# Optimization experiments

Hardware: AMD Instinct MI355X
Metric: run time of the kernel (lower is better)

The kernel has to match this reference:

```python
import jax, jax.numpy as jnp
import numpy as np

N_HEAD = 16
D_MODEL = 1024
D_K = 64
D_V = 64
LN_EPS = 1e-5


def setup_inputs() -> dict:
    key = jax.random.key(0)
    ks = jax.random.split(key, 12)
    B, S = 8, 1024
    q = jax.random.normal(ks[0], (B, S, D_MODEL), jnp.float32)
    k = jax.random.normal(ks[1], (B, S, D_MODEL), jnp.float32)
    v = jax.random.normal(ks[2], (B, S, D_MODEL), jnp.float32)
    mask = jnp.zeros((B, S, S), jnp.bool_)
    std_qk = np.sqrt(2.0 / (D_MODEL + D_K)).astype(np.float32)
    std_v = np.sqrt(2.0 / (D_MODEL + D_V)).astype(np.float32)
    Wq = jax.random.normal(ks[3], (D_MODEL, N_HEAD * D_K), jnp.float32) * std_qk
    Wk = jax.random.normal(ks[4], (D_MODEL, N_HEAD * D_K), jnp.float32) * std_qk
    Wv = jax.random.normal(ks[5], (D_MODEL, N_HEAD * D_V), jnp.float32) * std_v
    bq = jnp.zeros((N_HEAD * D_K,), jnp.float32)
    bk = jnp.zeros((N_HEAD * D_K,), jnp.float32)
    bv = jnp.zeros((N_HEAD * D_V,), jnp.float32)
    Wo = jax.random.normal(ks[6], (N_HEAD * D_V, D_MODEL), jnp.float32) * np.sqrt(2.0 / (N_HEAD * D_V + D_MODEL)).astype(np.float32)
    bo = jnp.zeros((D_MODEL,), jnp.float32)
    gamma = jnp.ones((D_MODEL,), jnp.float32)
    beta = jnp.zeros((D_MODEL,), jnp.float32)
    return {"q": q, "k": k, "v": v, "mask": mask, "Wq": Wq, "bq": bq,
            "Wk": Wk, "bk": bk, "Wv": Wv, "bv": bv, "Wo": Wo, "bo": bo,
            "gamma": gamma, "beta": beta}


def reference(q, k, v, mask, Wq, bq, Wk, bk, Wv, bv, Wo, bo, gamma, beta):
    B, Lq, _ = q.shape
    Lk = k.shape[1]
    residual = q
    # QKV projections -> (B, L, H, dh)
    qh = (q @ Wq + bq).reshape(B, Lq, N_HEAD, D_K)
    kh = (k @ Wk + bk).reshape(B, Lk, N_HEAD, D_K)
    vh = (v @ Wv + bv).reshape(B, Lk, N_HEAD, D_V)
    temperature = jnp.sqrt(jnp.asarray(D_K, qh.dtype))
    # scores: (H, B, Lq, Lk) to match torch head-major (n_head*bsz) layout
    scores = jnp.einsum('bqhd,bkhd->hbqk', qh, kh) / temperature
    scores = jnp.where(mask[None, :, :, :], -jnp.inf, scores)
    attn = jax.nn.softmax(scores, axis=-1)  # dropout is identity in eval
    out = jnp.einsum('hbqk,bkhd->bqhd', attn, vh).reshape(B, Lq, N_HEAD * D_V)
    out = out @ Wo + bo  # output dropout identity in eval
    # layer norm over last dim with residual
    x = out + residual
    mu = jnp.mean(x, axis=-1, keepdims=True)
    var = jnp.var(x, axis=-1, keepdims=True)
    y = (x - mu) * jax.lax.rsqrt(var + LN_EPS) * gamma + beta
    return y, attn.reshape(N_HEAD * B, Lq, Lk)
```

## Files before the change

kernel.cpp:

```cpp
#include <hip/hip_runtime.h>
#include <cstdint>

using f4  = __attribute__((ext_vector_type(4))) float;
using s8v = __attribute__((ext_vector_type(8))) short;
using u4v = __attribute__((ext_vector_type(4))) unsigned short;
using u8v = __attribute__((ext_vector_type(8))) unsigned short;

typedef unsigned short ushort_t;
typedef unsigned int   uint_t;

__device__ __forceinline__ ushort_t f2bf(float f) {
  union { float f; uint_t u; } x; x.f = f;
  uint_t r = x.u + 0x7fffu + ((x.u >> 16) & 1u);
  return (ushort_t)(r >> 16);
}
__device__ __forceinline__ float bf2f(ushort_t h) {
  union { uint_t u; float f; } x; x.u = ((uint_t)h) << 16;
  return x.f;
}

__device__ __forceinline__ void gload16(const void* gptr, void* ldsptr) {
  __builtin_amdgcn_global_load_lds(
      (const __attribute__((address_space(1))) void*)gptr,
      (__attribute__((address_space(3))) void*)ldsptr, 16, 0, 0);
}

__device__ __forceinline__ s8v ldfrag(const ushort_t* lds, int row, int kh, int g) {
  int cb = ((kh * 64 + g * 16) ^ ((row & 7) << 4));
  return *(const s8v*)((const char*)lds + row * 128 + cb);
}
__device__ __forceinline__ void st_p(ushort_t* lds, int row, int colbyte, ushort_t v) {
  *(ushort_t*)((char*)lds + row * 128 + (colbyte ^ ((row & 7) << 4))) = v;
}

__global__ __launch_bounds__(256) void wtrans_k(
    const float* __restrict__ Wq, const float* __restrict__ Wk,
    const float* __restrict__ Wv, const float* __restrict__ Wo,
    ushort_t* __restrict__ WT)
{
  int z = blockIdx.z;
  const float* W = (z == 0) ? Wq : (z == 1) ? Wk : (z == 2) ? Wv : Wo;
  ushort_t* D = WT + (size_t)z * 1048576;
  int k0 = blockIdx.x * 64, n0 = blockIdx.y * 64;
  __shared__ float t[64][65];
  int tid = threadIdx.x;
  int r16 = tid >> 4, c4 = (tid & 15) * 4;
#pragma unroll
  for (int p = 0; p < 4; ++p) {
    int kk = p * 16 + r16;
    f4 vv = *(const f4*)(W + (size_t)(k0 + kk) * 1024 + n0 + c4);
#pragma unroll
    for (int j = 0; j < 4; ++j) t[kk][c4 + j] = vv[j];
  }
  __syncthreads();
#pragma unroll
  for (int p = 0; p < 4; ++p) {
    int nn = p * 16 + r16;
    u4v o;
#pragma unroll
    for (int j = 0; j < 4; ++j) o[j] = f2bf(t[c4 + j][nn]);
    *(u4v*)(D + (size_t)(n0 + nn) * 1024 + k0 + c4) = o;
  }
}

__global__ __launch_bounds__(256) void gemm3_k(
    const float* __restrict__ Aq, const float* __restrict__ Ak,
    const float* __restrict__ Av, const ushort_t* __restrict__ WTall,
    const float* __restrict__ bq, const float* __restrict__ bk,
    const float* __restrict__ bv,
    ushort_t* __restrict__ Qh, ushort_t* __restrict__ Kh, ushort_t* __restrict__ Vh)
{
  __shared__ ushort_t As[128 * 64];
  __shared__ ushort_t Bs[128 * 64];
  int z = blockIdx.z;
  const float* A     = (z == 0) ? Aq : (z == 1) ? Ak : Av;
  const ushort_t* BT = WTall + (size_t)z * 1048576;
  const float* bias  = (z == 0) ? bq : (z == 1) ? bk : bv;
  ushort_t* out      = (z == 0) ? Qh : (z == 1) ? Kh : Vh;

  int tid = threadIdx.x;
  int l = tid & 63, w = tid >> 6;
  int lr = l & 15, g = l >> 4;
  int wr = w >> 1, wc = w & 1;
  const int m0 = blockIdx.x * 128;
  const int n0 = blockIdx.y * 128;

  f4 acc[4][4];
#pragma unroll
  for (int i = 0; i < 4; ++i)
#pragma unroll
    for (int j = 0; j < 4; ++j) acc[i][j] = (f4){0.f, 0.f, 0.f, 0.f};

  const ushort_t* Bp = BT + (size_t)n0 * 1024;
  const int swz = ((l & 7) ^ (l >> 3)) * 8;
  const int rb = l >> 3;

  for (int k0 = 0; k0 < 1024; k0 += 64) {
    __syncthreads();
#pragma unroll
    for (int c = 0; c < 4; ++c) {
      int seg = c * 4 + w;
      gload16(Bp + (size_t)(seg * 8 + rb) * 1024 + k0 + swz, (void*)(Bs + seg * 512));
    }
#pragma unroll
    for (int c = 0; c < 4; ++c) {
      int seg = c * 4 + w;
      int row = seg * 8 + rb;
      const float* ap = A + (size_t)(m0 + row) * 1024 + k0 + swz;
      f4 a0 = *(const f4*)ap;
      f4 a1 = *(const f4*)(ap + 4);
      u8v o;
      o[0] = f2bf(a0[0]); o[1] = f2bf(a0[1]); o[2] = f2bf(a0[2]); o[3] = f2bf(a0[3]);
      o[4] = f2bf(a1[0]); o[5] = f2bf(a1[1]); o[6] = f2bf(a1[2]); o[7] = f2bf(a1[3]);
      *(u8v*)((char*)As + row * 128 + (l & 7) * 16) = o;
    }
    __syncthreads();
#pragma unroll
    for (int kh = 0; kh < 2; ++kh) {
      s8v af[4], bfr[4];
#pragma unroll
      for (int mt = 0; mt < 4; ++mt) af[mt] = ldfrag(As, wr * 64 + mt * 16 + lr, kh, g);
#pragma unroll
      for (int nt = 0; nt < 4; ++nt) bfr[nt] = ldfrag(Bs, wc * 64 + nt * 16 + lr, kh, g);
#pragma unroll
      for (int mt = 0; mt < 4; ++mt)
#pragma unroll
        for (int nt = 0; nt < 4; ++nt)
          acc[mt][nt] = __builtin_amdgcn_mfma_f32_16x16x32_bf16(af[mt], bfr[nt], acc[mt][nt], 0, 0, 0);
    }
  }

#pragma unroll
  for (int nt = 0; nt < 4; ++nt) {
    int col = n0 + wc * 64 + nt * 16 + lr;
    float bvv = bias[col];
#pragma unroll
    for (int mt = 0; mt < 4; ++mt) {
#pragma unroll
      for (int r = 0; r < 4; ++r) {
        int row = m0 + wr * 64 + mt * 16 + g * 4 + r;
        float v = acc[mt][nt][r] + bvv;
        int b = row >> 10, s = row & 1023;
        int h = col >> 6, d = col & 63;
        size_t idx = (((size_t)b * 16 + h) * 1024 + s) * 64 + d;
        out[idx] = f2bf(v);
      }
    }
  }
}

__global__ __launch_bounds__(256) void gemmo_k(
    const ushort_t* __restrict__ A, const ushort_t* __restrict__ BT,
    const float* __restrict__ bias, ushort_t* __restrict__ out)
{
  __shared__ ushort_t As[128 * 64];
  __shared__ ushort_t Bs[128 * 64];
  int tid = threadIdx.x;
  int l = tid & 63, w = tid >> 6;
  int lr = l & 15, g = l >> 4;
  int wr = w >> 1, wc = w & 1;
  const int m0 = blockIdx.x * 128;
  const int n0 = blockIdx.y * 128;

  f4 acc[4][4];
#pragma unroll
  for (int i = 0; i < 4; ++i)
#pragma unroll
    for (int j = 0; j < 4; ++j) acc[i][j] = (f4){0.f, 0.f, 0.f, 0.f};

  const ushort_t* Ap = A + (size_t)m0 * 1024;
  const ushort_t* Bp = BT + (size_t)n0 * 1024;
  const int swz = ((l & 7) ^ (l >> 3)) * 8;
  const int rb = l >> 3;

  for (int k0 = 0; k0 < 1024; k0 += 64) {
    __syncthreads();
#pragma unroll
    for (int c = 0; c < 4; ++c) {
      int seg = c * 4 + w;
      gload16(Ap + (size_t)(seg * 8 + rb) * 1024 + k0 + swz, (void*)(As + seg * 512));
      gload16(Bp + (size_t)(seg * 8 + rb) * 1024 + k0 + swz, (void*)(Bs + seg * 512));
    }
    __syncthreads();
#pragma unroll
    for (int kh = 0; kh < 2; ++kh) {
      s8v af[4], bfr[4];
#pragma unroll
      for (int mt = 0; mt < 4; ++mt) af[mt] = ldfrag(As, wr * 64 + mt * 16 + lr, kh, g);
#pragma unroll
      for (int nt = 0; nt < 4; ++nt) bfr[nt] = ldfrag(Bs, wc * 64 + nt * 16 + lr, kh, g);
#pragma unroll
      for (int mt = 0; mt < 4; ++mt)
#pragma unroll
        for (int nt = 0; nt < 4; ++nt)
          acc[mt][nt] = __builtin_amdgcn_mfma_f32_16x16x32_bf16(af[mt], bfr[nt], acc[mt][nt], 0, 0, 0);
    }
  }

#pragma unroll
  for (int nt = 0; nt < 4; ++nt) {
    int col = n0 + wc * 64 + nt * 16 + lr;
    float bvv = bias[col];
#pragma unroll
    for (int mt = 0; mt < 4; ++mt) {
#pragma unroll
      for (int r = 0; r < 4; ++r) {
        int row = m0 + wr * 64 + mt * 16 + g * 4 + r;
        out[(size_t)row * 1024 + col] = f2bf(acc[mt][nt][r] + bvv);
      }
    }
  }
}

__global__ __launch_bounds__(256) void vtrans_k(const ushort_t* __restrict__ Vh,
                                                ushort_t* __restrict__ VhT)
{
  int bh = blockIdx.y, s0 = blockIdx.x * 64;
  __shared__ ushort_t t[64][72];
  int tid = threadIdx.x;
  const ushort_t* src = Vh + (size_t)bh * 65536;
  int ss = tid >> 2, d0 = (tid & 3) * 16;
#pragma unroll
  for (int c = 0; c < 2; ++c) {
    s8v vv = *(const s8v*)(src + (size_t)(s0 + ss) * 64 + d0 + c * 8);
    *(s8v*)&t[ss][d0 + c * 8] = vv;
  }
  __syncthreads();
  int d = tid >> 2, sc0 = (tid & 3) * 16;
  ushort_t* dst = VhT + (size_t)bh * 65536 + (size_t)d * 1024 + s0 + sc0;
  u8v o0, o1;
#pragma unroll
  for (int j = 0; j < 8; ++j) o0[j] = t[sc0 + j][d];
#pragma unroll
  for (int j = 0; j < 8; ++j) o1[j] = t[sc0 + 8 + j][d];
  *(u8v*)(dst) = o0;
  *(u8v*)(dst + 8) = o1;
}

__global__ __launch_bounds__(256) void attn_k(
    const ushort_t* __restrict__ Qh, const ushort_t* __restrict__ Kh,
    const ushort_t* __restrict__ VhT, float* __restrict__ attn,
    ushort_t* __restrict__ Oh)
{
  __shared__ ushort_t sh[4 * 64 * 64];
  ushort_t* Qs = sh;
  ushort_t* Ks = sh + 4096;
  ushort_t* Vs = sh + 8192;
  ushort_t* Ps = sh + 12288;
  int tid = threadIdx.x;
  int l = tid & 63, w = tid >> 6;
  int lr = l & 15, g = l >> 4;
  int lin = blockIdx.y * 16 + blockIdx.x;
  int swzb = (lin & 7) * 256 + (lin >> 3);
  int bh = swzb >> 4;
  int q0 = (swzb & 15) * 64;
  int b = bh >> 4, h = bh & 15;
  const ushort_t* Qb = Qh + (size_t)bh * 65536 + (size_t)q0 * 64;
  const ushort_t* Kb = Kh + (size_t)bh * 65536;
  const ushort_t* Vb = VhT + (size_t)bh * 65536;
  float* ab = attn + (((size_t)(h * 8 + b)) * 1024 + q0) * 1024;

  const int swz = ((l & 7) ^ (l >> 3)) * 8;
  const int rb = l >> 3;

#pragma unroll
  for (int c = 0; c < 2; ++c) {
    int seg = c * 4 + w;
    gload16(Qb + (size_t)(seg * 8 + rb) * 64 + swz, (void*)(Qs + seg * 512));
  }

  float ls[4] = {0.f, 0.f, 0.f, 0.f};
  f4 acc[4];
#pragma unroll
  for (int nt = 0; nt < 4; ++nt) acc[nt] = (f4){0.f, 0.f, 0.f, 0.f};

  for (int kv0 = 0; kv0 < 1024; kv0 += 64) {
    __syncthreads();
#pragma unroll
    for (int c = 0; c < 2; ++c) {
      int seg = c * 4 + w;
      gload16(Kb + (size_t)(kv0 + seg * 8 + rb) * 64 + swz, (void*)(Ks + seg * 512));
      gload16(Vb + (size_t)(seg * 8 + rb) * 1024 + kv0 + swz, (void*)(Vs + seg * 512));
    }
    __syncthreads();
    s8v qa0 = ldfrag(Qs, w * 16 + lr, 0, g);
    s8v qa1 = ldfrag(Qs, w * 16 + lr, 1, g);
    float pv[4][4];
    __builtin_amdgcn_s_setprio(1);
#pragma unroll
    for (int nt = 0; nt < 4; ++nt) {
      s8v kf0 = ldfrag(Ks, nt * 16 + lr, 0, g);
      s8v kf1 = ldfrag(Ks, nt * 16 + lr, 1, g);
      f4 z = (f4){0.f, 0.f, 0.f, 0.f};
      z = __builtin_amdgcn_mfma_f32_16x16x32_bf16(qa0, kf0, z, 0, 0, 0);
      z = __builtin_amdgcn_mfma_f32_16x16x32_bf16(qa1, kf1, z, 0, 0, 0);
#pragma unroll
      for (int r = 0; r < 4; ++r) pv[nt][r] = __expf(z[r] * 0.125f);
    }
    __builtin_amdgcn_s_setprio(0);
#pragma unroll
    for (int r = 0; r < 4; ++r) {
      float ps = (pv[0][r] + pv[1][r]) + (pv[2][r] + pv[3][r]);
      ps += __shfl_xor(ps, 1);
      ps += __shfl_xor(ps, 2);
      ps += __shfl_xor(ps, 4);
      ps += __shfl_xor(ps, 8);
      ls[r] += ps;
    }
#pragma unroll
    for (int nt = 0; nt < 4; ++nt)
#pragma unroll
      for (int r = 0; r < 4; ++r)
        st_p(Ps, w * 16 + g * 4 + r, (nt * 16 + lr) * 2, f2bf(pv[nt][r]));
    s8v p0 = ldfrag(Ps, w * 16 + lr, 0, g);
    s8v p1 = ldfrag(Ps, w * 16 + lr, 1, g);
    __builtin_amdgcn_s_setprio(1);
#pragma unroll
    for (int nt = 0; nt < 4; ++nt) {
      s8v v0 = ldfrag(Vs, nt * 16 + lr, 0, g);
      s8v v1 = ldfrag(Vs, nt * 16 + lr, 1, g);
      acc[nt] = __builtin_amdgcn_mfma_f32_16x16x32_bf16(p0, v0, acc[nt], 0, 0, 0);
      acc[nt] = __builtin_amdgcn_mfma_f32_16x16x32_bf16(p1, v1, acc[nt], 0, 0, 0);
    }
    __builtin_amdgcn_s_setprio(0);
  }

  float rl[4];
#pragma unroll
  for (int r = 0; r < 4; ++r) rl[r] = 1.f / ls[r];

  __syncthreads();
  float* Lf = (float*)(sh + 4096);
  s8v qb0 = ldfrag(Qs, w * 16 + lr, 0, g);
  s8v qb1 = ldfrag(Qs, w * 16 + lr, 1, g);
  for (int kv0 = 0; kv0 < 1024; kv0 += 64) {
    f4 z[4];
#pragma unroll
    for (int nt = 0; nt < 4; ++nt) {
      const ushort_t* kp = Kb + (size_t)(kv0 + nt * 16 + lr) * 64;
      s8v kf0 = *(const s8v*)(kp + g * 8);
      s8v kf1 = *(const s8v*)(kp + 32 + g * 8);
      f4 zz = (f4){0.f, 0.f, 0.f, 0.f};
      zz = __builtin_amdgcn_mfma_f32_16x16x32_bf16(qb0, kf0, zz, 0, 0, 0);
      zz = __builtin_amdgcn_mfma_f32_16x16x32_bf16(qb1, kf1, zz, 0, 0, 0);
      z[nt] = zz;
    }
#pragma unroll
    for (int r = 0; r < 4; ++r) {
#pragma unroll
      for (int nt = 0; nt < 4; ++nt)
        Lf[w * 272 + g * 68 + nt * 16 + lr] = __expf(z[nt][r] * 0.125f) * rl[r];
      f4 o = *(const f4*)&Lf[w * 272 + g * 68 + lr * 4];
      __builtin_nontemporal_store(
          o, (f4*)(ab + (size_t)(w * 16 + g * 4 + r) * 1024 + kv0 + lr * 4));
    }
  }

#pragma unroll
  for (int nt = 0; nt < 4; ++nt) {
#pragma unroll
    for (int r = 0; r < 4; ++r) {
      int s = q0 + w * 16 + g * 4 + r;
      size_t idx = (((size_t)b * 1024 + s) * 16 + h) * 64 + nt * 16 + lr;
      Oh[idx] = f2bf(acc[nt][r] * rl[r]);
    }
  }
}

__global__ __launch_bounds__(256) void ln_k(
    const ushort_t* __restrict__ OUT, const float* __restrict__ res,
    const float* __restrict__ gamma, const float* __restrict__ beta,
    float* __restrict__ y)
{
  int row = blockIdx.x;
  int tid = threadIdx.x;
  int l = tid & 63, w = tid >> 6;
  size_t base = (size_t)row * 1024 + tid * 4;
  u4v ov = *(const u4v*)(OUT + base);
  f4 rv = *(const f4*)(res + base);
  float x0 = bf2f(ov[0]) + rv[0];
  float x1 = bf2f(ov[1]) + rv[1];
  float x2 = bf2f(ov[2]) + rv[2];
  float x3 = bf2f(ov[3]) + rv[3];
  float s1 = x0 + x1 + x2 + x3;
  float s2 = x0 * x0 + x1 * x1 + x2 * x2 + x3 * x3;
#pragma unroll
  for (int off = 1; off < 64; off <<= 1) {
    s1 += __shfl_xor(s1, off);
    s2 += __shfl_xor(s2, off);
  }
  __shared__ float r1[4], r2[4];
  if (l == 0) { r1[w] = s1; r2[w] = s2; }
  __syncthreads();
  float tot = r1[0] + r1[1] + r1[2] + r1[3];
  float tot2 = r2[0] + r2[1] + r2[2] + r2[3];
  float mu = tot * (1.f / 1024.f);
  float var = tot2 * (1.f / 1024.f) - mu * mu;
  float rs = rsqrtf(var + 1e-5f);
  f4 gv = *(const f4*)(gamma + tid * 4);
  f4 bv = *(const f4*)(beta + tid * 4);
  f4 o;
  o[0] = (x0 - mu) * rs * gv[0] + bv[0];
  o[1] = (x1 - mu) * rs * gv[1] + bv[1];
  o[2] = (x2 - mu) * rs * gv[2] + bv[2];
  o[3] = (x3 - mu) * rs * gv[3] + bv[3];
  *(f4*)(y + base) = o;
}

extern "C" void kernel_launch(void* const* d_in, const int* in_sizes, int n_in,
                              void* d_out, int out_size, void* d_ws, size_t ws_size,
                              hipStream_t stream) {
  const float* q     = (const float*)d_in[0];
  const float* k     = (const float*)d_in[1];
  const float* v     = (const float*)d_in[2];
  const float* Wq    = (const float*)d_in[4];
  const float* bq    = (const float*)d_in[5];
  const float* Wk    = (const float*)d_in[6];
  const float* bk    = (const float*)d_in[7];
  const float* Wv    = (const float*)d_in[8];
  const float* bv    = (const float*)d_in[9];
  const float* Wo    = (const float*)d_in[10];
  const float* bo    = (const float*)d_in[11];
  const float* gamma = (const float*)d_in[12];
  const float* beta  = (const float*)d_in[13];

  float* y    = (float*)d_out;
  float* attn = y + 8388608;

  char* ws = (char*)d_ws;
  ushort_t* WT  = (ushort_t*)ws;
  ushort_t* Qh  = (ushort_t*)(ws + 8388608);
  ushort_t* Kh  = Qh + 8388608;
  ushort_t* Vh  = Kh + 8388608;
  ushort_t* VhT = Vh + 8388608;
  ushort_t* Oh  = VhT + 8388608;
  ushort_t* OUT = Oh + 8388608;

  wtrans_k<<<dim3(16, 16, 4), 256, 0, stream>>>(Wq, Wk, Wv, Wo, WT);
  gemm3_k<<<dim3(64, 8, 3), 256, 0, stream>>>(q, k, v, WT, bq, bk, bv, Qh, Kh, Vh);
  vtrans_k<<<dim3(16, 128), 256, 0, stream>>>(Vh, VhT);
  attn_k<<<dim3(16, 128), 256, 0, stream>>>(Qh, Kh, VhT, attn, Oh);
  gemmo_k<<<dim3(64, 8), 256, 0, stream>>>(Oh, WT + 3145728, bo, OUT);
  ln_k<<<8192, 256, 0, stream>>>(OUT, q, gamma, beta, y);
}
```

Measured before the change: 325.4 us.

## Compute transposed QK^T so P feeds PV MFMA directly from registers

Swaps the MFMA operand order for the score computation so each lane holds a full row of P values, letting the bf16 P fragments be packed in registers instead of round-tripping through LDS. Row sums become a two-step cross-group shuffle rather than a four-step butterfly. V fragments are now gathered from four 8-byte LDS reads to match the new P layout, and Q fragments are hoisted out of the loop. The second pass writes probabilities row-wise into the staging buffer with vector stores. This trades LDS scalar stores and a sync-free P round trip for more, smaller LDS reads on V.

```diff
diff --git a/kernel.cpp b/kernel.cpp
--- a/kernel.cpp
+++ b/kernel.cpp
@@ -3,6 +3,7 @@
 
 using f4  = __attribute__((ext_vector_type(4))) float;
 using s8v = __attribute__((ext_vector_type(8))) short;
+using s4v = __attribute__((ext_vector_type(4))) short;
 using u4v = __attribute__((ext_vector_type(4))) unsigned short;
 using u8v = __attribute__((ext_vector_type(8))) unsigned short;
 
@@ -29,8 +30,9 @@
   int cb = ((kh * 64 + g * 16) ^ ((row & 7) << 4));
   return *(const s8v*)((const char*)lds + row * 128 + cb);
 }
-__device__ __forceinline__ void st_p(ushort_t* lds, int row, int colbyte, ushort_t v) {
-  *(ushort_t*)((char*)lds + row * 128 + (colbyte ^ ((row & 7) << 4))) = v;
+__device__ __forceinline__ s4v ldv64(const ushort_t* lds, int row, int cb) {
+  int p = (cb ^ ((row & 7) << 4));
+  return *(const s4v*)((const char*)lds + row * 128 + p);
 }
 
 __global__ __launch_bounds__(256) void wtrans_k(
@@ -242,11 +244,10 @@
     const ushort_t* __restrict__ VhT, float* __restrict__ attn,
     ushort_t* __restrict__ Oh)
 {
-  __shared__ ushort_t sh[4 * 64 * 64];
+  __shared__ ushort_t sh[12800];
   ushort_t* Qs = sh;
   ushort_t* Ks = sh + 4096;
   ushort_t* Vs = sh + 8192;
-  ushort_t* Ps = sh + 12288;
   int tid = threadIdx.x;
   int l = tid & 63, w = tid >> 6;
   int lr = l & 15, g = l >> 4;
@@ -268,8 +269,11 @@
     int seg = c * 4 + w;
     gload16(Qb + (size_t)(seg * 8 + rb) * 64 + swz, (void*)(Qs + seg * 512));
   }
-
-  float ls[4] = {0.f, 0.f, 0.f, 0.f};
+  __syncthreads();
+  s8v qa0 = ldfrag(Qs, w * 16 + lr, 0, g);
+  s8v qa1 = ldfrag(Qs, w * 16 + lr, 1, g);
+
+  float ls = 0.f;
   f4 acc[4];
 #pragma unroll
   for (int nt = 0; nt < 4; ++nt) acc[nt] = (f4){0.f, 0.f, 0.f, 0.f};
@@ -283,56 +287,63 @@
       gload16(Vb + (size_t)(seg * 8 + rb) * 1024 + kv0 + swz, (void*)(Vs + seg * 512));
     }
     __syncthreads();
-    s8v qa0 = ldfrag(Qs, w * 16 + lr, 0, g);
-    s8v qa1 = ldfrag(Qs, w * 16 + lr, 1, g);
-    float pv[4][4];
+    f4 z[4];
     __builtin_amdgcn_s_setprio(1);
 #pragma unroll
     for (int nt = 0; nt < 4; ++nt) {
       s8v kf0 = ldfrag(Ks, nt * 16 + lr, 0, g);
       s8v kf1 = ldfrag(Ks, nt * 16 + lr, 1, g);
-      f4 z = (f4){0.f, 0.f, 0.f, 0.f};
-      z = __builtin_amdgcn_mfma_f32_16x16x32_bf16(qa0, kf0, z, 0, 0, 0);
-      z = __builtin_amdgcn_mfma_f32_16x16x32_bf16(qa1, kf1, z, 0, 0, 0);
-#pragma unroll
-      for (int r = 0; r < 4; ++r) pv[nt][r] = __expf(z[r] * 0.125f);
+      f4 zz = (f4){0.f, 0.f, 0.f, 0.f};
+      zz = __builtin_amdgcn_mfma_f32_16x16x32_bf16(kf0, qa0, zz, 0, 0, 0);
+      zz = __builtin_amdgcn_mfma_f32_16x16x32_bf16(kf1, qa1, zz, 0, 0, 0);
+      z[nt] = zz;
     }
     __builtin_amdgcn_s_setprio(0);
-#pragma unroll
-    for (int r = 0; r < 4; ++r) {
-      float ps = (pv[0][r] + pv[1][r]) + (pv[2][r] + pv[3][r]);
-      ps += __shfl_xor(ps, 1);
-      ps += __shfl_xor(ps, 2);
-      ps += __shfl_xor(ps, 4);
-      ps += __shfl_xor(ps, 8);
-      ls[r] += ps;
-    }
+    float pv[4][4];
+    float psum = 0.f;
 #pragma unroll
     for (int nt = 0; nt < 4; ++nt)
 #pragma unroll
-      for (int r = 0; r < 4; ++r)
-        st_p(Ps, w * 16 + g * 4 + r, (nt * 16 + lr) * 2, f2bf(pv[nt][r]));
-    s8v p0 = ldfrag(Ps, w * 16 + lr, 0, g);
-    s8v p1 = ldfrag(Ps, w * 16 + lr, 1, g);
+      for (int r = 0; r < 4; ++r) {
+        pv[nt][r] = __expf(z[nt][r] * 0.125f);
+        psum += pv[nt][r];
+      }
+    psum += __shfl_xor(psum, 16);
+    psum += __shfl_xor(psum, 32);
+    ls += psum;
+    u8v pu0, pu1;
+#pragma unroll
+    for (int j = 0; j < 4; ++j) {
+      pu0[j]     = f2bf(pv[0][j]);
+      pu0[j + 4] = f2bf(pv[1][j]);
+      pu1[j]     = f2bf(pv[2][j]);
+      pu1[j + 4] = f2bf(pv[3][j]);
+    }
+    s8v pa0 = *(s8v*)&pu0;
+    s8v pa1 = *(s8v*)&pu1;
     __builtin_amdgcn_s_setprio(1);
 #pragma unroll
     for (int nt = 0; nt < 4; ++nt) {
-      s8v v0 = ldfrag(Vs, nt * 16 + lr, 0, g);
-      s8v v1 = ldfrag(Vs, nt * 16 + lr, 1, g);
-      acc[nt] = __builtin_amdgcn_mfma_f32_16x16x32_bf16(p0, v0, acc[nt], 0, 0, 0);
-      acc[nt] = __builtin_amdgcn_mfma_f32_16x16x32_bf16(p1, v1, acc[nt], 0, 0, 0);
+      int d = nt * 16 + lr;
+      s4v a0 = ldv64(Vs, d, 8 * g);
+      s4v a1 = ldv64(Vs, d, 32 + 8 * g);
+      s4v a2 = ldv64(Vs, d, 64 + 8 * g);
+      s4v a3 = ldv64(Vs, d, 96 + 8 * g);
+      s8v vb0 = (s8v){a0[0], a0[1], a0[2], a0[3], a1[0], a1[1], a1[2], a1[3]};
+      s8v vb1 = (s8v){a2[0], a2[1], a2[2], a2[3], a3[0], a3[1], a3[2], a3[3]};
+      acc[nt] = __builtin_amdgcn_mfma_f32_16x16x32_bf16(pa0, vb0, acc[nt], 0, 0, 0);
+      acc[nt] = __builtin_amdgcn_mfma_f32_16x16x32_bf16(pa1, vb1, acc[nt], 0, 0, 0);
     }
     __builtin_amdgcn_s_setprio(0);
   }
 
+  float rlocal = 1.f / ls;
   float rl[4];
 #pragma unroll
-  for (int r = 0; r < 4; ++r) rl[r] = 1.f / ls[r];
+  for (int r = 0; r < 4; ++r) rl[r] = __shfl(rlocal, g * 4 + r);
 
   __syncthreads();
   float* Lf = (float*)(sh + 4096);
-  s8v qb0 = ldfrag(Qs, w * 16 + lr, 0, g);
-  s8v qb1 = ldfrag(Qs, w * 16 + lr, 1, g);
   for (int kv0 = 0; kv0 < 1024; kv0 += 64) {
     f4 z[4];
 #pragma unroll
@@ -341,16 +352,20 @@
       s8v kf0 = *(const s8v*)(kp + g * 8);
       s8v kf1 = *(const s8v*)(kp + 32 + g * 8);
       f4 zz = (f4){0.f, 0.f, 0.f, 0.f};
-      zz = __builtin_amdgcn_mfma_f32_16x16x32_bf16(qb0, kf0, zz, 0, 0, 0);
-      zz = __builtin_amdgcn_mfma_f32_16x16x32_bf16(qb1, kf1, zz, 0, 0, 0);
+      zz = __builtin_amdgcn_mfma_f32_16x16x32_bf16(kf0, qa0, zz, 0, 0, 0);
+      zz = __builtin_amdgcn_mfma_f32_16x16x32_bf16(kf1, qa1, zz, 0, 0, 0);
       z[nt] = zz;
     }
 #pragma unroll
+    for (int nt = 0; nt < 4; ++nt) {
+      f4 o;
+#pragma unroll
+      for (int r = 0; r < 4; ++r) o[r] = __expf(z[nt][r] * 0.125f) * rlocal;
+      *(f4*)&Lf[(w * 16 + lr) * 68 + nt * 16 + g * 4] = o;
+    }
+#pragma unroll
     for (int r = 0; r < 4; ++r) {
-#pragma unroll
-      for (int nt = 0; nt < 4; ++nt)
-        Lf[w * 272 + g * 68 + nt * 16 + lr] = __expf(z[nt][r] * 0.125f) * rl[r];
-      f4 o = *(const f4*)&Lf[w * 272 + g * 68 + lr * 4];
+      f4 o = *(const f4*)&Lf[(w * 16 + g * 4 + r) * 68 + lr * 4];
       __builtin_nontemporal_store(
           o, (f4*)(ab + (size_t)(w * 16 + g * 4 + r) * 1024 + kv0 + lr * 4));
     }
```

Measured after the change: 312.6 us (median of 2 runs). -3.9%, faster.
